# Kernel tuning notes

Hardware: AMD Instinct MI355X
Metric: run time of the kernel (lower is better)

## Reference

```python
import jax, jax.numpy as jnp
import numpy as np

B, C, D = 16384, 4096, 256

def setup_inputs() -> dict:
    key = jax.random.key(0)
    k1, k2, k3 = jax.random.split(key, 3)
    z = jax.random.normal(k1, (B, D), dtype=jnp.float32)
    mu = jax.random.normal(k2, (C, D), dtype=jnp.float32)
    logvar = jax.random.normal(k3, (C, D), dtype=jnp.float32)
    return {"z": z, "mu": mu, "logvar": logvar}

def reference(z, mu, logvar):
    # Vectorized form of the per-class loop in _approx_class_probabilities.
    # log_gauss(z; mu_c, logvar_c) = -0.5*(sum_d((z-mu_c)^2/var_c + logvar_c) + D*log(2pi))
    # Expand (z-mu)^2/var = z^2/var - 2*z*mu/var + mu^2/var so the sum over d
    # becomes three [B,D]x[D,C] contractions (no [B,C,D] intermediate).
    d = z.shape[1]
    num_classes = mu.shape[0]
    log_prior = jnp.float32(np.log(1.0 / num_classes))
    inv_var = jnp.exp(-logvar)                                   # [C, D]
    quad = (jnp.einsum('bd,cd->bc', z * z, inv_var)
            - 2.0 * jnp.einsum('bd,cd->bc', z, mu * inv_var)
            + jnp.sum(mu * mu * inv_var, axis=1)[None, :])       # [B, C]
    logvar_sum = jnp.sum(logvar, axis=1)[None, :]                # [1, C]
    class_logits = -0.5 * (quad + logvar_sum + d * jnp.float32(np.log(2 * np.pi))) + log_prior
    class_prob = jax.nn.softmax(class_logits, axis=1)
    predicted_classes = jnp.argmax(class_prob, axis=1)
    return class_logits, class_prob, predicted_classes
```

## Files before the change

### kernel.cpp

```cpp
#include <hip/hip_runtime.h>
#include <math.h>


constexpr int M = 16384;
constexpr int N = 4096;
constexpr int DD = 256;
constexpr int K = 1536;
constexpr int BM = 128, BN = 128, BK = 64;

typedef _Float16 half_t;
typedef __attribute__((ext_vector_type(8))) _Float16 half8;
typedef __attribute__((ext_vector_type(4))) float floatx4;

#define GLOBAL_AS(p) ((const __attribute__((address_space(1))) void*)(p))
#define LDS_AS(p) ((__attribute__((address_space(3))) void*)(p))

__global__ __launch_bounds__(256) void prep_w_kernel(const float* __restrict__ mu,
                                                     const float* __restrict__ logvar,
                                                     half_t* __restrict__ Wt,
                                                     float* __restrict__ Kc) {
    const int c = blockIdx.x;
    const int d = threadIdx.x;
    const float lv = logvar[(size_t)c * DD + d];
    const float m  = mu[(size_t)c * DD + d];
    const float iv = __expf(-lv);
    const float w1 = -0.5f * iv;
    const float w2 = m * iv;
    const half_t w1h = (half_t)w1;
    const half_t w1l = (half_t)(w1 - (float)w1h);
    const half_t w2h = (half_t)w2;
    const half_t w2l = (half_t)(w2 - (float)w2h);
    half_t* row = Wt + (size_t)c * K;
    row[d]        = w1h;
    row[256 + d]  = w2h;
    row[512 + d]  = w1l;
    row[768 + d]  = w2l;
    row[1024 + d] = w1h;
    row[1280 + d] = w2h;

    float s = m * m * iv + lv;
    #pragma unroll
    for (int off = 32; off > 0; off >>= 1) s += __shfl_down(s, off, 64);
    __shared__ float ls[4];
    const int lane = threadIdx.x & 63, wvi = threadIdx.x >> 6;
    if (lane == 0) ls[wvi] = s;
    __syncthreads();
    if (threadIdx.x == 0) {
        const float t = ls[0] + ls[1] + ls[2] + ls[3];
        Kc[c] = -0.5f * t - 235.24826450039618f - 8.31776616671934f;
    }
}

__global__ __launch_bounds__(256) void prep_a_kernel(const float* __restrict__ z,
                                                     half_t* __restrict__ At) {
    const int b = blockIdx.x;
    const int d = threadIdx.x;
    const float zv = z[(size_t)b * DD + d];
    const float z2 = zv * zv;
    const half_t z2h = (half_t)z2;
    const half_t z2l = (half_t)(z2 - (float)z2h);
    const half_t zh  = (half_t)zv;
    const half_t zl  = (half_t)(zv - (float)zh);
    half_t* row = At + (size_t)b * K;
    row[d]        = z2h;
    row[256 + d]  = zh;
    row[512 + d]  = z2h;
    row[768 + d]  = zh;
    row[1024 + d] = z2l;
    row[1280 + d] = zl;
}

__global__ __launch_bounds__(256) void gemm_kernel(const half_t* __restrict__ At,
                                                   const half_t* __restrict__ Wt,
                                                   const float* __restrict__ Kc,
                                                   float* __restrict__ logits) {
    __shared__ half_t As[BM * BK];
    __shared__ half_t Bs[BN * BK];

    const int bn0 = blockIdx.x * BN;
    const int bm0 = blockIdx.y * BM;
    const int tid = threadIdx.x;
    const int lane = tid & 63;
    const int wvi = tid >> 6;
    const int wm = (wvi & 1) * 64;
    const int wn = (wvi >> 1) * 64;
    const int quad = lane >> 4;
    const int l15 = lane & 15;

    const int r0 = tid >> 3;
    const int cl = ((tid & 7) ^ (r0 & 7)) * 8;
    const char* gA = (const char*)(At + (size_t)(bm0 + r0) * K + cl);
    const char* gB = (const char*)(Wt + (size_t)(bn0 + r0) * K + cl);
    char* lA = (char*)As + tid * 16;
    char* lB = (char*)Bs + tid * 16;

    floatx4 acc[4][4] = {};

    for (int kt = 0; kt < K / BK; ++kt) {
        const size_t kb = (size_t)kt * BK * 2;
        #pragma unroll
        for (int i = 0; i < 4; ++i) {
            __builtin_amdgcn_global_load_lds(GLOBAL_AS(gA + kb + (size_t)i * 32 * K * 2),
                                             LDS_AS(lA + i * 4096), 16, 0, 0);
            __builtin_amdgcn_global_load_lds(GLOBAL_AS(gB + kb + (size_t)i * 32 * K * 2),
                                             LDS_AS(lB + i * 4096), 16, 0, 0);
        }
        __syncthreads();
        #pragma unroll
        for (int ks = 0; ks < 2; ++ks) {
            half8 af[4], bf[4];
            #pragma unroll
            for (int mi = 0; mi < 4; ++mi) {
                const int m = wm + mi * 16 + l15;
                const int c8 = (ks * 4 + quad) ^ (m & 7);
                af[mi] = *(const half8*)(As + m * BK + c8 * 8);
            }
            #pragma unroll
            for (int ni = 0; ni < 4; ++ni) {
                const int n = wn + ni * 16 + l15;
                const int c8 = (ks * 4 + quad) ^ (n & 7);
                bf[ni] = *(const half8*)(Bs + n * BK + c8 * 8);
            }
            #pragma unroll
            for (int mi = 0; mi < 4; ++mi)
                #pragma unroll
                for (int ni = 0; ni < 4; ++ni)
                    acc[mi][ni] = __builtin_amdgcn_mfma_f32_16x16x32_f16(
                        af[mi], bf[ni], acc[mi][ni], 0, 0, 0);
        }
        __syncthreads();
    }

    float kc[4];
    #pragma unroll
    for (int ni = 0; ni < 4; ++ni) kc[ni] = Kc[bn0 + wn + ni * 16 + l15];
    #pragma unroll
    for (int mi = 0; mi < 4; ++mi) {
        const int row0 = bm0 + wm + mi * 16 + quad * 4;
        #pragma unroll
        for (int ni = 0; ni < 4; ++ni) {
            const int col = bn0 + wn + ni * 16 + l15;
            float* outp = logits + (size_t)row0 * N + col;
            #pragma unroll
            for (int r = 0; r < 4; ++r)
                outp[(size_t)r * N] = acc[mi][ni][r] + kc[ni];
        }
    }
}

__global__ __launch_bounds__(256) void softmax_kernel(const float* __restrict__ logits,
                                                      float* __restrict__ probs,
                                                      float* __restrict__ pred) {
    const int row = blockIdx.x;
    const int tid = threadIdx.x;
    const int lane = tid & 63, wvi = tid >> 6;
    const float4* lrow = (const float4*)(logits + (size_t)row * N);
    float4 v[4];
    float vmax = -INFINITY;
    int vidx = 0;
    #pragma unroll
    for (int j = 0; j < 4; ++j) {
        v[j] = lrow[j * 256 + tid];
        const int base = (j * 256 + tid) * 4;
        if (v[j].x > vmax) { vmax = v[j].x; vidx = base; }
        if (v[j].y > vmax) { vmax = v[j].y; vidx = base + 1; }
        if (v[j].z > vmax) { vmax = v[j].z; vidx = base + 2; }
        if (v[j].w > vmax) { vmax = v[j].w; vidx = base + 3; }
    }
    #pragma unroll
    for (int off = 32; off > 0; off >>= 1) {
        const float ov = __shfl_down(vmax, off, 64);
        const int oi = __shfl_down(vidx, off, 64);
        if (ov > vmax || (ov == vmax && oi < vidx)) { vmax = ov; vidx = oi; }
    }
    __shared__ float smax[4];
    __shared__ int sidx[4];
    __shared__ float ssum[4];
    if (lane == 0) { smax[wvi] = vmax; sidx[wvi] = vidx; }
    __syncthreads();
    float rmax = smax[0];
    int ridx = sidx[0];
    #pragma unroll
    for (int i = 1; i < 4; ++i)
        if (smax[i] > rmax || (smax[i] == rmax && sidx[i] < ridx)) { rmax = smax[i]; ridx = sidx[i]; }

    float s = 0.f;
    float4 e[4];
    #pragma unroll
    for (int j = 0; j < 4; ++j) {
        e[j].x = __expf(v[j].x - rmax);
        e[j].y = __expf(v[j].y - rmax);
        e[j].z = __expf(v[j].z - rmax);
        e[j].w = __expf(v[j].w - rmax);
        s += e[j].x + e[j].y + e[j].z + e[j].w;
    }
    #pragma unroll
    for (int off = 32; off > 0; off >>= 1) s += __shfl_down(s, off, 64);
    if (lane == 0) ssum[wvi] = s;
    __syncthreads();
    const float inv = 1.f / (ssum[0] + ssum[1] + ssum[2] + ssum[3]);
    float4* prow = (float4*)(probs + (size_t)row * N);
    #pragma unroll
    for (int j = 0; j < 4; ++j) {
        float4 o;
        o.x = e[j].x * inv; o.y = e[j].y * inv; o.z = e[j].z * inv; o.w = e[j].w * inv;
        prow[j * 256 + tid] = o;
    }
    if (tid == 0) pred[row] = (float)ridx;
}

extern "C" void kernel_launch(void* const* d_in, const int* in_sizes, int n_in,
                              void* d_out, int out_size, void* d_ws, size_t ws_size,
                              hipStream_t stream) {
    const float* z      = (const float*)d_in[0];
    const float* mu     = (const float*)d_in[1];
    const float* logvar = (const float*)d_in[2];
    float* out    = (float*)d_out;
    float* logits = out;
    float* probs  = out + (size_t)M * N;
    float* pred   = out + (size_t)2 * M * N;

    char* scratch = (char*)probs;
    half_t* At = (half_t*)scratch;
    half_t* Wt = (half_t*)(scratch + (size_t)M * K * 2);
    float*  Kc = (float*)(scratch + (size_t)M * K * 2 + (size_t)N * K * 2);

    prep_w_kernel<<<N, 256, 0, stream>>>(mu, logvar, Wt, Kc);
    prep_a_kernel<<<M, 256, 0, stream>>>(z, At);
    gemm_kernel<<<dim3(N / BN, M / BM), 256, 0, stream>>>(At, Wt, Kc, logits);
    softmax_kernel<<<M, 256, 0, stream>>>(logits, probs, pred);
}
```

Baseline: 779.3 us.

## Stage GEMM epilogue through LDS, vectorize prep kernels, use wave-per-row softmax

The GEMM epilogue now writes accumulators into shared memory in two halves and stores the logits tile to global memory as coalesced float4 rows, instead of scattered 4-byte stores. The prep kernels now handle one row per wavefront with float4 loads and half4 stores. The softmax kernel maps one row to each wavefront and uses xor-shuffle reductions with no shared memory or block barriers. The epilogue adds two barriers and LDS traffic, and the softmax holds 64 floats per thread in registers.

```diff
diff --git a/kernel.cpp b/kernel.cpp
--- a/kernel.cpp
+++ b/kernel.cpp
@@ -4,11 +4,11 @@
 
 constexpr int M = 16384;
 constexpr int N = 4096;
-constexpr int DD = 256;
 constexpr int K = 1536;
 constexpr int BM = 128, BN = 128, BK = 64;
 
 typedef _Float16 half_t;
+typedef __attribute__((ext_vector_type(4))) _Float16 half4;
 typedef __attribute__((ext_vector_type(8))) _Float16 half8;
 typedef __attribute__((ext_vector_type(4))) float floatx4;
 
@@ -19,63 +19,68 @@
                                                      const float* __restrict__ logvar,
                                                      half_t* __restrict__ Wt,
                                                      float* __restrict__ Kc) {
-    const int c = blockIdx.x;
-    const int d = threadIdx.x;
-    const float lv = logvar[(size_t)c * DD + d];
-    const float m  = mu[(size_t)c * DD + d];
-    const float iv = __expf(-lv);
-    const float w1 = -0.5f * iv;
-    const float w2 = m * iv;
-    const half_t w1h = (half_t)w1;
-    const half_t w1l = (half_t)(w1 - (float)w1h);
-    const half_t w2h = (half_t)w2;
-    const half_t w2l = (half_t)(w2 - (float)w2h);
-    half_t* row = Wt + (size_t)c * K;
-    row[d]        = w1h;
-    row[256 + d]  = w2h;
-    row[512 + d]  = w1l;
-    row[768 + d]  = w2l;
-    row[1024 + d] = w1h;
-    row[1280 + d] = w2h;
-
-    float s = m * m * iv + lv;
-    #pragma unroll
-    for (int off = 32; off > 0; off >>= 1) s += __shfl_down(s, off, 64);
-    __shared__ float ls[4];
-    const int lane = threadIdx.x & 63, wvi = threadIdx.x >> 6;
-    if (lane == 0) ls[wvi] = s;
-    __syncthreads();
-    if (threadIdx.x == 0) {
-        const float t = ls[0] + ls[1] + ls[2] + ls[3];
-        Kc[c] = -0.5f * t - 235.24826450039618f - 8.31776616671934f;
-    }
+    const int tid = threadIdx.x;
+    const int lane = tid & 63, wvi = tid >> 6;
+    const int c = blockIdx.x * 4 + wvi;
+    const float4 m4 = ((const float4*)mu)[(size_t)c * 64 + lane];
+    const float4 l4 = ((const float4*)logvar)[(size_t)c * 64 + lane];
+    const float mm[4] = {m4.x, m4.y, m4.z, m4.w};
+    const float lv[4] = {l4.x, l4.y, l4.z, l4.w};
+    half4 w1h, w1l, w2h, w2l;
+    float s = 0.f;
+    #pragma unroll
+    for (int i = 0; i < 4; ++i) {
+        const float iv = __expf(-lv[i]);
+        const float w1 = -0.5f * iv;
+        const float w2 = mm[i] * iv;
+        w1h[i] = (half_t)w1; w1l[i] = (half_t)(w1 - (float)w1h[i]);
+        w2h[i] = (half_t)w2; w2l[i] = (half_t)(w2 - (float)w2h[i]);
+        s += mm[i] * mm[i] * iv + lv[i];
+    }
+    half4* row = (half4*)(Wt + (size_t)c * K);
+    row[lane]       = w1h;
+    row[64 + lane]  = w2h;
+    row[128 + lane] = w1l;
+    row[192 + lane] = w2l;
+    row[256 + lane] = w1h;
+    row[320 + lane] = w2h;
+    #pragma unroll
+    for (int off = 1; off < 64; off <<= 1) s += __shfl_xor(s, off, 64);
+    if (lane == 0)
+        Kc[c] = -0.5f * s - 235.24826450039618f - 8.31776616671934f;
 }
 
 __global__ __launch_bounds__(256) void prep_a_kernel(const float* __restrict__ z,
                                                      half_t* __restrict__ At) {
-    const int b = blockIdx.x;
-    const int d = threadIdx.x;
-    const float zv = z[(size_t)b * DD + d];
-    const float z2 = zv * zv;
-    const half_t z2h = (half_t)z2;
-    const half_t z2l = (half_t)(z2 - (float)z2h);
-    const half_t zh  = (half_t)zv;
-    const half_t zl  = (half_t)(zv - (float)zh);
-    half_t* row = At + (size_t)b * K;
-    row[d]        = z2h;
-    row[256 + d]  = zh;
-    row[512 + d]  = z2h;
-    row[768 + d]  = zh;
-    row[1024 + d] = z2l;
-    row[1280 + d] = zl;
+    const int tid = threadIdx.x;
+    const int lane = tid & 63, wvi = tid >> 6;
+    const int b = blockIdx.x * 4 + wvi;
+    const float4 z4 = ((const float4*)z)[(size_t)b * 64 + lane];
+    const float zv[4] = {z4.x, z4.y, z4.z, z4.w};
+    half4 z2h, z2l, zh, zl;
+    #pragma unroll
+    for (int i = 0; i < 4; ++i) {
+        const float z2 = zv[i] * zv[i];
+        z2h[i] = (half_t)z2; z2l[i] = (half_t)(z2 - (float)z2h[i]);
+        zh[i]  = (half_t)zv[i]; zl[i] = (half_t)(zv[i] - (float)zh[i]);
+    }
+    half4* row = (half4*)(At + (size_t)b * K);
+    row[lane]       = z2h;
+    row[64 + lane]  = zh;
+    row[128 + lane] = z2h;
+    row[192 + lane] = zh;
+    row[256 + lane] = z2l;
+    row[320 + lane] = zl;
 }
 
 __global__ __launch_bounds__(256) void gemm_kernel(const half_t* __restrict__ At,
                                                    const half_t* __restrict__ Wt,
                                                    const float* __restrict__ Kc,
                                                    float* __restrict__ logits) {
-    __shared__ half_t As[BM * BK];
-    __shared__ half_t Bs[BN * BK];
+    __shared__ char smem[BM * BK * 2 + BN * BK * 2];
+    half_t* As = (half_t*)smem;
+    half_t* Bs = As + BM * BK;
+    float*  Cs = (float*)smem;
 
     const int bn0 = blockIdx.x * BN;
     const int bm0 = blockIdx.y * BM;
@@ -134,16 +139,31 @@
     float kc[4];
     #pragma unroll
     for (int ni = 0; ni < 4; ++ni) kc[ni] = Kc[bn0 + wn + ni * 16 + l15];
-    #pragma unroll
-    for (int mi = 0; mi < 4; ++mi) {
-        const int row0 = bm0 + wm + mi * 16 + quad * 4;
+
+    const int seg = tid & 31;
+    const int rg  = tid >> 5;
+    #pragma unroll
+    for (int h = 0; h < 2; ++h) {
+        __syncthreads();
+        if ((wvi & 1) == h) {
+            #pragma unroll
+            for (int mi = 0; mi < 4; ++mi) {
+                const int lr = mi * 16 + quad * 4;
+                #pragma unroll
+                for (int ni = 0; ni < 4; ++ni) {
+                    const int lc = wn + ni * 16 + l15;
+                    #pragma unroll
+                    for (int r = 0; r < 4; ++r)
+                        Cs[(lr + r) * 128 + lc] = acc[mi][ni][r] + kc[ni];
+                }
+            }
+        }
+        __syncthreads();
         #pragma unroll
-        for (int ni = 0; ni < 4; ++ni) {
-            const int col = bn0 + wn + ni * 16 + l15;
-            float* outp = logits + (size_t)row0 * N + col;
-            #pragma unroll
-            for (int r = 0; r < 4; ++r)
-                outp[(size_t)r * N] = acc[mi][ni][r] + kc[ni];
+        for (int i = 0; i < 8; ++i) {
+            const int lr = i * 8 + rg;
+            const float4 val = *(const float4*)(Cs + lr * 128 + seg * 4);
+            *(float4*)(logits + (size_t)(bm0 + h * 64 + lr) * N + bn0 + seg * 4) = val;
         }
     }
 }
@@ -151,62 +171,48 @@
 __global__ __launch_bounds__(256) void softmax_kernel(const float* __restrict__ logits,
                                                       float* __restrict__ probs,
                                                       float* __restrict__ pred) {
-    const int row = blockIdx.x;
     const int tid = threadIdx.x;
     const int lane = tid & 63, wvi = tid >> 6;
+    const int row = blockIdx.x * 4 + wvi;
     const float4* lrow = (const float4*)(logits + (size_t)row * N);
-    float4 v[4];
+    float4 v[16];
     float vmax = -INFINITY;
     int vidx = 0;
     #pragma unroll
-    for (int j = 0; j < 4; ++j) {
-        v[j] = lrow[j * 256 + tid];
-        const int base = (j * 256 + tid) * 4;
+    for (int j = 0; j < 16; ++j) {
+        v[j] = lrow[j * 64 + lane];
+        const int base = (j * 64 + lane) * 4;
         if (v[j].x > vmax) { vmax = v[j].x; vidx = base; }
         if (v[j].y > vmax) { vmax = v[j].y; vidx = base + 1; }
         if (v[j].z > vmax) { vmax = v[j].z; vidx = base + 2; }
         if (v[j].w > vmax) { vmax = v[j].w; vidx = base + 3; }
     }
     #pragma unroll
-    for (int off = 32; off > 0; off >>= 1) {
-        const float ov = __shfl_down(vmax, off, 64);
-        const int oi = __shfl_down(vidx, off, 64);
+    for (int off = 1; off < 64; off <<= 1) {
+        const float ov = __shfl_xor(vmax, off, 64);
+        const int oi = __shfl_xor(vidx, off, 64);
         if (ov > vmax || (ov == vmax && oi < vidx)) { vmax = ov; vidx = oi; }
     }
-    __shared__ float smax[4];
-    __shared__ int sidx[4];
-    __shared__ float ssum[4];
-    if (lane == 0) { smax[wvi] = vmax; sidx[wvi] = vidx; }
-    __syncthreads();
-    float rmax = smax[0];
-    int ridx = sidx[0];
-    #pragma unroll
-    for (int i = 1; i < 4; ++i)
-        if (smax[i] > rmax || (smax[i] == rmax && sidx[i] < ridx)) { rmax = smax[i]; ridx = sidx[i]; }
-
     float s = 0.f;
-    float4 e[4];
-    #pragma unroll
-    for (int j = 0; j < 4; ++j) {
-        e[j].x = __expf(v[j].x - rmax);
-        e[j].y = __expf(v[j].y - rmax);
-        e[j].z = __expf(v[j].z - rmax);
-        e[j].w = __expf(v[j].w - rmax);
-        s += e[j].x + e[j].y + e[j].z + e[j].w;
-    }
-    #pragma unroll
-    for (int off = 32; off > 0; off >>= 1) s += __shfl_down(s, off, 64);
-    if (lane == 0) ssum[wvi] = s;
-    __syncthreads();
-    const float inv = 1.f / (ssum[0] + ssum[1] + ssum[2] + ssum[3]);
+    #pragma unroll
+    for (int j = 0; j < 16; ++j) {
+        v[j].x = __expf(v[j].x - vmax);
+        v[j].y = __expf(v[j].y - vmax);
+        v[j].z = __expf(v[j].z - vmax);
+        v[j].w = __expf(v[j].w - vmax);
+        s += v[j].x + v[j].y + v[j].z + v[j].w;
+    }
+    #pragma unroll
+    for (int off = 1; off < 64; off <<= 1) s += __shfl_xor(s, off, 64);
+    const float inv = 1.f / s;
     float4* prow = (float4*)(probs + (size_t)row * N);
     #pragma unroll
-    for (int j = 0; j < 4; ++j) {
+    for (int j = 0; j < 16; ++j) {
         float4 o;
-        o.x = e[j].x * inv; o.y = e[j].y * inv; o.z = e[j].z * inv; o.w = e[j].w * inv;
-        prow[j * 256 + tid] = o;
-    }
-    if (tid == 0) pred[row] = (float)ridx;
+        o.x = v[j].x * inv; o.y = v[j].y * inv; o.z = v[j].z * inv; o.w = v[j].w * inv;
+        prow[j * 64 + lane] = o;
+    }
+    if (lane == 0) pred[row] = (float)vidx;
 }
 
 extern "C" void kernel_launch(void* const* d_in, const int* in_sizes, int n_in,
@@ -225,8 +231,8 @@
     half_t* Wt = (half_t*)(scratch + (size_t)M * K * 2);
     float*  Kc = (float*)(scratch + (size_t)M * K * 2 + (size_t)N * K * 2);
 
-    prep_w_kernel<<<N, 256, 0, stream>>>(mu, logvar, Wt, Kc);
-    prep_a_kernel<<<M, 256, 0, stream>>>(z, At);
+    prep_w_kernel<<<N / 4, 256, 0, stream>>>(mu, logvar, Wt, Kc);
+    prep_a_kernel<<<M / 4, 256, 0, stream>>>(z, At);
     gemm_kernel<<<dim3(N / BN, M / BM), 256, 0, stream>>>(At, Wt, Kc, logits);
-    softmax_kernel<<<M, 256, 0, stream>>>(logits, probs, pred);
-}
+    softmax_kernel<<<M / 4, 256, 0, stream>>>(logits, probs, pred);
+}
```

Result: slower. 815.7 us (+4.7%).
